# Kernel optimization log

Measured on AMD Instinct MI355X. Metric: run time of the kernel, lower is better.

The kernel has to match this reference:

```python
import jax, jax.numpy as jnp
import numpy as np

N_HEAD = 32
N_KV_HEAD = 8
HD = 64  # head dim
N_EMBD = 2048
B, T = 2, 2048
ROPE_THETA = 10000.0


def _apply_rope(x, cos, sin):
    # x: [B, T, H, HD]; cos/sin: [T, HD//2]. Interleaved complex pairs (even, odd),
    # matching torch.view_as_complex on x.reshape(..., -1, 2).
    x0 = x[..., 0::2]
    x1 = x[..., 1::2]
    c = cos[None, :, None, :]
    s = sin[None, :, None, :]
    o0 = x0 * c - x1 * s
    o1 = x0 * s + x1 * c
    return jnp.stack([o0, o1], axis=-1).reshape(x.shape)


def setup_inputs() -> dict:
    key = jax.random.key(0)
    k1, k2, k3 = jax.random.split(key, 3)
    x = jax.random.normal(k1, (B, T, N_EMBD), dtype=jnp.float32)
    Wqkv = jax.random.normal(k2, ((N_HEAD + 2 * N_KV_HEAD) * HD, N_EMBD), dtype=jnp.float32) * 0.02
    Wproj = jax.random.normal(k3, (N_EMBD, N_EMBD), dtype=jnp.float32) * 0.02
    # precompute_freqs_cis as in llm.c (llama path)
    freqs = 1.0 / (ROPE_THETA ** (np.arange(0, HD, 2, dtype=np.float32) / HD))
    ang = np.outer(np.arange(T, dtype=np.float32), freqs)  # [T, HD//2]
    freqs_cos = jnp.asarray(np.cos(ang), dtype=jnp.float32)
    freqs_sin = jnp.asarray(np.sin(ang), dtype=jnp.float32)
    return {"x": x, "Wqkv": Wqkv, "Wproj": Wproj,
            "freqs_cos": freqs_cos, "freqs_sin": freqs_sin, "start_pos": -1}


def reference(x, Wqkv, Wproj, freqs_cos, freqs_sin, start_pos):
    Bx, Tx, C = x.shape
    n_rep = N_HEAD // N_KV_HEAD
    qkv = x @ Wqkv.T  # [B, T, (H + 2*KV)*HD]
    q = qkv[..., : N_HEAD * HD].reshape(Bx, Tx, N_HEAD, HD)
    k = qkv[..., N_HEAD * HD: (N_HEAD + N_KV_HEAD) * HD].reshape(Bx, Tx, N_KV_HEAD, HD)
    v = qkv[..., (N_HEAD + N_KV_HEAD) * HD:].reshape(Bx, Tx, N_KV_HEAD, HD)
    # RoPE on q, k
    q = _apply_rope(q, freqs_cos, freqs_sin)
    k = _apply_rope(k, freqs_cos, freqs_sin)
    # start_pos < 0: training path, no KV cache. GQA repeat of kv heads.
    k = jnp.repeat(k, n_rep, axis=2)  # [B, T, H, HD]
    v = jnp.repeat(v, n_rep, axis=2)
    q = q.transpose(0, 2, 1, 3)  # [B, H, T, HD]
    k = k.transpose(0, 2, 1, 3)
    v = v.transpose(0, 2, 1, 3)
    scale = 1.0 / np.sqrt(HD).astype(np.float32)
    scores = jnp.einsum("bhtd,bhsd->bhts", q, k) * scale  # [B, H, T, T]
    causal = jnp.tril(jnp.ones((Tx, Tx), dtype=bool))
    scores = jnp.where(causal[None, None, :, :], scores, -jnp.inf)
    att = jax.nn.softmax(scores.astype(jnp.float32), axis=-1).astype(q.dtype)
    y = jnp.einsum("bhts,bhsd->bhtd", att, v)
    y = y.transpose(0, 2, 1, 3).reshape(Bx, Tx, C)
    return y @ Wproj.T
```

## Files before the change

### kernel.cpp

```cpp
#include <hip/hip_runtime.h>
#include <hip/hip_bf16.h>
#include <cstdint>

#define NH   32
#define NKV  8
#define HD   64
#define CE   2048
#define BB   2
#define TT   2048
#define QKVD 3072
#define MM   (BB*TT)

typedef float  f32x4  __attribute__((ext_vector_type(4)));
typedef float  f32x16 __attribute__((ext_vector_type(16)));
typedef short  s16x8  __attribute__((ext_vector_type(8)));
typedef unsigned short u16;

#define AS1 __attribute__((address_space(1)))
#define AS3 __attribute__((address_space(3)))
#define GLDS16(src, dst) __builtin_amdgcn_global_load_lds( \
    (const AS1 uint32_t*)(src), (AS3 uint32_t*)(dst), 16, 0, 0)

static __device__ __forceinline__ float bf2f(u16 u) {
    union { uint32_t u; float f; } v; v.u = ((uint32_t)u) << 16; return v.f;
}
static __device__ __forceinline__ u16 f2bf(float f) {
    union { float f; uint32_t u; } v; v.f = f;
    uint32_t r = v.u + 0x7fffu + ((v.u >> 16) & 1u);
    return (u16)(r >> 16);
}
static __device__ __forceinline__ uint32_t cvtpk(float lo, float hi) {
    uint32_t r;
    asm("v_cvt_pk_bf16_f32 %0, %1, %2" : "=v"(r) : "v"(lo), "v"(hi));
    return r;
}
static __device__ __forceinline__ void plswap(uint32_t &a, uint32_t &b) {
    asm volatile("v_permlane32_swap_b32 %0, %1" : "+v"(a), "+v"(b));
}

__global__ void k_f32_to_bf16(const float* __restrict__ in, uint32_t* __restrict__ out, int n8) {
    int i = blockIdx.x * blockDim.x + threadIdx.x;
    if (i >= n8) return;
    const float4* p = reinterpret_cast<const float4*>(in) + (size_t)i * 2;
    float4 a = p[0], b = p[1];
    uint4 o;
    o.x = cvtpk(a.x, a.y); o.y = cvtpk(a.z, a.w);
    o.z = cvtpk(b.x, b.y); o.w = cvtpk(b.z, b.w);
    *reinterpret_cast<uint4*>(out + (size_t)i * 4) = o;
}

template<bool OUT_BF16>
__global__ __launch_bounds__(256) void k_gemm_bt(const u16* __restrict__ A,
                                                 const u16* __restrict__ Bm,
                                                 void* __restrict__ Cout,
                                                 int M, int N, int K) {
    __shared__ u16 As[128 * 32];
    __shared__ u16 Bs[128 * 32];
    const int tid  = threadIdx.x;
    const int m0   = blockIdx.y * 128;
    const int n0   = blockIdx.x * 128;
    const int w    = tid >> 6;
    const int lane = tid & 63;
    const int lr   = lane & 15, lg = lane >> 4;
    const int wm   = (w >> 1) * 64, wn = (w & 1) * 64;

    const int o0 = w * 2048 + lane * 16, o1 = o0 + 1024;
    const int ar0 = o0 >> 6, ar1 = o1 >> 6;
    const int ac0 = (o0 & 63) >> 1, ac1 = (o1 & 63) >> 1;
    const size_t aof0 = (size_t)(m0 + ar0) * K + ac0;
    const size_t aof1 = (size_t)(m0 + ar1) * K + ac1;
    const size_t bof0 = (size_t)(n0 + ar0) * K + ac0;
    const size_t bof1 = (size_t)(n0 + ar1) * K + ac1;
    u16* dA0 = &As[w * 1024];       u16* dA1 = &As[w * 1024 + 512];
    u16* dB0 = &Bs[w * 1024];       u16* dB1 = &Bs[w * 1024 + 512];

    f32x4 acc[4][4] = {};

    for (int k0 = 0; k0 < K; k0 += 32) {
        GLDS16(A  + aof0 + k0, dA0);
        GLDS16(A  + aof1 + k0, dA1);
        GLDS16(Bm + bof0 + k0, dB0);
        GLDS16(Bm + bof1 + k0, dB1);
        __syncthreads();
        s16x8 af[4], bf[4];
        #pragma unroll
        for (int i = 0; i < 4; ++i)
            af[i] = *reinterpret_cast<const s16x8*>(&As[(wm + i * 16 + lr) * 32 + lg * 8]);
        #pragma unroll
        for (int j = 0; j < 4; ++j)
            bf[j] = *reinterpret_cast<const s16x8*>(&Bs[(wn + j * 16 + lr) * 32 + lg * 8]);
        #pragma unroll
        for (int i = 0; i < 4; ++i)
            #pragma unroll
            for (int j = 0; j < 4; ++j)
                acc[i][j] = __builtin_amdgcn_mfma_f32_16x16x32_bf16(af[i], bf[j], acc[i][j], 0, 0, 0);
        __syncthreads();
    }

    #pragma unroll
    for (int i = 0; i < 4; ++i)
        #pragma unroll
        for (int j = 0; j < 4; ++j)
            #pragma unroll
            for (int r = 0; r < 4; ++r) {
                int m = m0 + wm + i * 16 + lg * 4 + r;
                int n = n0 + wn + j * 16 + lr;
                if constexpr (OUT_BF16)
                    reinterpret_cast<u16*>(Cout)[(size_t)m * N + n] = f2bf(acc[i][j][r]);
                else
                    reinterpret_cast<float*>(Cout)[(size_t)m * N + n] = acc[i][j][r];
            }
}

__global__ void k_rope_scatter(const u16* __restrict__ qkv,
                               const float* __restrict__ fcos,
                               const float* __restrict__ fsin,
                               u16* __restrict__ Q,
                               u16* __restrict__ Kb,
                               u16* __restrict__ Vt) {
    int p = blockIdx.x * blockDim.x + threadIdx.x;
    if (p >= MM * (QKVD / 2)) return;
    int row = p / (QKVD / 2);
    int f   = (p % (QKVD / 2)) * 2;
    int b = row / TT, t = row % TT;
    uint32_t pk = reinterpret_cast<const uint32_t*>(qkv)[(size_t)row * (QKVD / 2) + (f >> 1)];
    u16 u0 = (u16)(pk & 0xffff), u1 = (u16)(pk >> 16);
    const float QS = 0.18033688011112042f;
    if (f < NH * HD) {
        int h = f / HD, d = f % HD;
        float c = fcos[t * 32 + (d >> 1)], s = fsin[t * 32 + (d >> 1)];
        float x0 = bf2f(u0), x1 = bf2f(u1);
        uint32_t o = cvtpk((x0 * c - x1 * s) * QS, (x0 * s + x1 * c) * QS);
        *reinterpret_cast<uint32_t*>(Q + ((size_t)((b * NH + h) * TT + t)) * HD + d) = o;
    } else if (f < NH * HD + NKV * HD) {
        int fk = f - NH * HD;
        int h = fk / HD, d = fk % HD;
        float c = fcos[t * 32 + (d >> 1)], s = fsin[t * 32 + (d >> 1)];
        float x0 = bf2f(u0), x1 = bf2f(u1);
        uint32_t o = cvtpk(x0 * c - x1 * s, x0 * s + x1 * c);
        *reinterpret_cast<uint32_t*>(Kb + ((size_t)((b * NKV + h) * TT + t)) * HD + d) = o;
    } else {
        int fv = f - NH * HD - NKV * HD;
        int h = fv / HD, d = fv % HD;
        Vt[((size_t)(b * NKV + h) * HD + d) * TT + t]     = u0;
        Vt[((size_t)(b * NKV + h) * HD + d + 1) * TT + t] = u1;
    }
}

__global__ __launch_bounds__(256) void k_attn(const u16* __restrict__ Q,
                                              const u16* __restrict__ Kb,
                                              const u16* __restrict__ Vt,
                                              u16* __restrict__ Y) {
    __shared__ u16 Ks[2][4096];
    __shared__ u16 Vs[2][4096];

    const int tid = threadIdx.x;
    const int w = tid >> 6, lane = tid & 63;
    const int ql = lane & 31, hi = lane >> 5;
    const int hi16 = hi << 4;
    const int b = blockIdx.z, h = blockIdx.y, kvh = h >> 2;

    const u16* qbase = Q  + ((size_t)(b * NH  + h  ) * TT) * HD;
    const u16* kbase = Kb + ((size_t)(b * NKV + kvh) * TT) * HD;
    const u16* vbase = Vt + ((size_t)(b * NKV + kvh) * HD) * TT;

    const int o0 = w * 2048 + lane * 16, o1 = o0 + 1024;
    const int r0 = o0 >> 7, r1 = o1 >> 7;
    const int c0 = (o0 & 127) ^ ((r0 & 7) << 4);
    const int c1 = (o1 & 127) ^ ((r1 & 7) << 4);
    const size_t kof0 = (size_t)r0 * HD + (c0 >> 1);
    const size_t kof1 = (size_t)r1 * HD + (c1 >> 1);
    const size_t vof0 = (size_t)r0 * TT + (c0 >> 1);
    const size_t vof1 = (size_t)r1 * TT + (c1 >> 1);

    const char* KsB = (const char*)&Ks[0][0];
    const char* VsB = (const char*)&Vs[0][0];
    const int krb0 = (0 * 32 + ql) * 128, ksz0 = ((0 * 32 + ql) & 7) << 4;
    const int krb1 = (1 * 32 + ql) * 128, ksz1 = ((1 * 32 + ql) & 7) << 4;

    #pragma unroll 1
    for (int pi = 0; pi < 2; ++pi) {
        const int j    = pi ? (int)blockIdx.x : (15 - (int)blockIdx.x);
        const int q0w  = j * 128 + w * 32;
        const int nt   = 2 * j + 2;
        const int tmxw = (q0w + 31) >> 6;
        const int qabs = q0w + ql;

        s16x8 qf[4];
        #pragma unroll
        for (int ds = 0; ds < 4; ++ds)
            qf[ds] = *reinterpret_cast<const s16x8*>(qbase + (size_t)qabs * HD + ds * 16 + 8 * hi);
        asm volatile("s_waitcnt vmcnt(0)" ::: "memory");

        GLDS16(kbase + kof0, &Ks[0][w * 1024]);
        GLDS16(kbase + kof1, &Ks[0][w * 1024 + 512]);
        GLDS16(vbase + vof0, &Vs[0][w * 1024]);
        GLDS16(vbase + vof1, &Vs[0][w * 1024 + 512]);

        float mrow = -1e30f, lrowp = 0.f;
        f32x16 oT0 = {}, oT1 = {};

        for (int t = 0; t < nt; ++t) {
            const int cur = t & 1;
            const int kv0 = t * 64;
            if (t + 1 < nt) {
                const size_t kb2 = (size_t)(kv0 + 64) * HD;
                GLDS16(kbase + kb2 + kof0, &Ks[cur ^ 1][w * 1024]);
                GLDS16(kbase + kb2 + kof1, &Ks[cur ^ 1][w * 1024 + 512]);
                GLDS16(vbase + (kv0 + 64) + vof0, &Vs[cur ^ 1][w * 1024]);
                GLDS16(vbase + (kv0 + 64) + vof1, &Vs[cur ^ 1][w * 1024 + 512]);
                asm volatile("s_waitcnt vmcnt(4)" ::: "memory");
            } else {
                asm volatile("s_waitcnt vmcnt(0)" ::: "memory");
            }
            __builtin_amdgcn_s_barrier();
            __builtin_amdgcn_sched_barrier(0);

            if (t <= tmxw) {
                const int bufo = cur * 8192;

                f32x16 sc0 = {}, sc1 = {};
                #pragma unroll
                for (int ds = 0; ds < 4; ++ds) {
                    s16x8 k0 = *reinterpret_cast<const s16x8*>(KsB + bufo + krb0 + (((ds << 5) | hi16) ^ ksz0));
                    s16x8 k1 = *reinterpret_cast<const s16x8*>(KsB + bufo + krb1 + (((ds << 5) | hi16) ^ ksz1));
                    sc0 = __builtin_amdgcn_mfma_f32_32x32x16_bf16(k0, qf[ds], sc0, 0, 0, 0);
                    sc1 = __builtin_amdgcn_mfma_f32_32x32x16_bf16(k1, qf[ds], sc1, 0, 0, 0);
                }

                float p0[16], p1[16];
                #pragma unroll
                for (int r = 0; r < 16; ++r) { p0[r] = sc0[r]; p1[r] = sc1[r]; }

                if (t == tmxw) {
                    const int dq = qabs - kv0 - 4 * hi;
                    #pragma unroll
                    for (int r = 0; r < 16; ++r) {
                        const int kr = (r & 3) + 8 * (r >> 2);
                        p0[r] = (kr      <= dq) ? p0[r] : -1e30f;
                        p1[r] = (kr + 32 <= dq) ? p1[r] : -1e30f;
                    }
                }

                float tmax = fmaxf(p0[0], p1[0]);
                #pragma unroll
                for (int r = 1; r < 16; ++r) tmax = fmaxf(tmax, fmaxf(p0[r], p1[r]));
                if (__any(tmax > mrow + 8.f)) {
                    float tf = fmaxf(tmax, __shfl_xor(tmax, 32, 64));
                    float mn = fmaxf(mrow, tf);
                    float alpha = __builtin_amdgcn_exp2f(mrow - mn);
                    mrow = mn;
                    lrowp *= alpha;
                    #pragma unroll
                    for (int r = 0; r < 16; ++r) { oT0[r] *= alpha; oT1[r] *= alpha; }
                }

                float sum = 0.f;
                #pragma unroll
                for (int r = 0; r < 16; ++r) {
                    p0[r] = __builtin_amdgcn_exp2f(p0[r] - mrow);
                    p1[r] = __builtin_amdgcn_exp2f(p1[r] - mrow);
                    sum += p0[r] + p1[r];
                }
                lrowp += sum;

                #pragma unroll
                for (int ks = 0; ks < 2; ++ks) {
                    uint32_t a0 = cvtpk(p0[ks * 8 + 0], p0[ks * 8 + 1]);
                    uint32_t b0 = cvtpk(p0[ks * 8 + 4], p0[ks * 8 + 5]);
                    plswap(a0, b0);
                    uint32_t a1 = cvtpk(p0[ks * 8 + 2], p0[ks * 8 + 3]);
                    uint32_t b1 = cvtpk(p0[ks * 8 + 6], p0[ks * 8 + 7]);
                    plswap(a1, b1);
                    union { uint32_t d[4]; s16x8 v; } pb;
                    pb.d[0] = a0; pb.d[1] = a1; pb.d[2] = b0; pb.d[3] = b1;
                    const int colb = (0 << 6) | (ks << 5) | hi16;
                    s16x8 v0 = *reinterpret_cast<const s16x8*>(VsB + bufo + krb0 + (colb ^ ksz0));
                    s16x8 v1 = *reinterpret_cast<const s16x8*>(VsB + bufo + krb1 + (colb ^ ksz1));
                    oT0 = __builtin_amdgcn_mfma_f32_32x32x16_bf16(v0, pb.v, oT0, 0, 0, 0);
                    oT1 = __builtin_amdgcn_mfma_f32_32x32x16_bf16(v1, pb.v, oT1, 0, 0, 0);
                }
                #pragma unroll
                for (int ks = 0; ks < 2; ++ks) {
                    uint32_t a0 = cvtpk(p1[ks * 8 + 0], p1[ks * 8 + 1]);
                    uint32_t b0 = cvtpk(p1[ks * 8 + 4], p1[ks * 8 + 5]);
                    plswap(a0, b0);
                    uint32_t a1 = cvtpk(p1[ks * 8 + 2], p1[ks * 8 + 3]);
                    uint32_t b1 = cvtpk(p1[ks * 8 + 6], p1[ks * 8 + 7]);
                    plswap(a1, b1);
                    union { uint32_t d[4]; s16x8 v; } pb;
                    pb.d[0] = a0; pb.d[1] = a1; pb.d[2] = b0; pb.d[3] = b1;
                    const int colb = (1 << 6) | (ks << 5) | hi16;
                    s16x8 v0 = *reinterpret_cast<const s16x8*>(VsB + bufo + krb0 + (colb ^ ksz0));
                    s16x8 v1 = *reinterpret_cast<const s16x8*>(VsB + bufo + krb1 + (colb ^ ksz1));
                    oT0 = __builtin_amdgcn_mfma_f32_32x32x16_bf16(v0, pb.v, oT0, 0, 0, 0);
                    oT1 = __builtin_amdgcn_mfma_f32_32x32x16_bf16(v1, pb.v, oT1, 0, 0, 0);
                }
            }

            __builtin_amdgcn_sched_barrier(0);
            __builtin_amdgcn_s_barrier();
        }

        lrowp += __shfl_xor(lrowp, 32, 64);
        const float rinv = 1.f / lrowp;
        const size_t yrow = ((size_t)(b * TT + qabs) * NH + h) * HD;
        #pragma unroll
        for (int rp = 0; rp < 8; ++rp) {
            const int d = ((2 * rp) & 3) + 8 * (rp >> 1) + 4 * hi;
            *reinterpret_cast<uint32_t*>(Y + yrow + d) =
                cvtpk(oT0[2 * rp] * rinv, oT0[2 * rp + 1] * rinv);
            *reinterpret_cast<uint32_t*>(Y + yrow + 32 + d) =
                cvtpk(oT1[2 * rp] * rinv, oT1[2 * rp + 1] * rinv);
        }
    }
}

extern "C" void kernel_launch(void* const* d_in, const int* in_sizes, int n_in,
                              void* d_out, int out_size, void* d_ws, size_t ws_size,
                              hipStream_t stream) {
    (void)in_sizes; (void)n_in; (void)out_size; (void)ws_size;
    const float* x     = (const float*)d_in[0];
    const float* wqkv  = (const float*)d_in[1];
    const float* wproj = (const float*)d_in[2];
    const float* fcos  = (const float*)d_in[3];
    const float* fsin  = (const float*)d_in[4];

    char* ws = (char*)d_ws;
    size_t off = 0;
    auto alloc = [&](size_t bytes) { void* p = ws + off; off += (bytes + 255) & ~(size_t)255; return p; };
    u16* Xbf  = (u16*)alloc((size_t)MM * CE * 2);
    u16* Wqb  = (u16*)alloc((size_t)QKVD * CE * 2);
    u16* Wpb  = (u16*)alloc((size_t)CE * CE * 2);
    u16* QKVb = (u16*)alloc((size_t)MM * QKVD * 2);
    u16* Qb   = (u16*)alloc((size_t)BB * NH * TT * HD * 2);
    u16* Kbuf = (u16*)alloc((size_t)BB * NKV * TT * HD * 2);
    u16* Vtb  = (u16*)alloc((size_t)BB * NKV * HD * TT * 2);
    u16* Yb   = (u16*)alloc((size_t)MM * CE * 2);

    k_f32_to_bf16<<<(MM * CE / 8 + 255) / 256, 256, 0, stream>>>(x, (uint32_t*)Xbf, MM * CE / 8);
    k_f32_to_bf16<<<(QKVD * CE / 8 + 255) / 256, 256, 0, stream>>>(wqkv, (uint32_t*)Wqb, QKVD * CE / 8);
    k_f32_to_bf16<<<(CE * CE / 8 + 255) / 256, 256, 0, stream>>>(wproj, (uint32_t*)Wpb, CE * CE / 8);

    dim3 g1(QKVD / 128, MM / 128);
    k_gemm_bt<true><<<g1, 256, 0, stream>>>(Xbf, Wqb, QKVb, MM, QKVD, CE);

    int pairs = MM * (QKVD / 2);
    k_rope_scatter<<<(pairs + 255) / 256, 256, 0, stream>>>(QKVb, fcos, fsin, Qb, Kbuf, Vtb);

    dim3 ga(8, NH, BB);
    k_attn<<<ga, 256, 0, stream>>>(Qb, Kbuf, Vtb, Yb);

    dim3 g2(CE / 128, MM / 128);
    k_gemm_bt<false><<<g2, 256, 0, stream>>>(Yb, Wpb, d_out, MM, CE, CE);
}
```

Measured before the change: 238.8 us.

## Fuse RoPE and QKV scatter into QKV GEMM epilogue, remap tiles, add setprio

Moves RoPE, Q scaling and the Q/K/Vt scatter into the epilogue of the QKV GEMM, which removes the intermediate QKV buffer and the separate rope/scatter kernel. Both GEMMs now remap block indices so that tiles sharing the same A rows run close together, for better L2 reuse. The attention kernel also wraps its MFMA sections in s_setprio so those waves get issue priority. The cost is an epilogue with lane shuffles and scattered cos/sin loads inside the GEMM.

```diff
diff --git a/kernel.cpp b/kernel.cpp
--- a/kernel.cpp
+++ b/kernel.cpp
@@ -49,16 +49,22 @@
     *reinterpret_cast<uint4*>(out + (size_t)i * 4) = o;
 }
 
-template<bool OUT_BF16>
-__global__ __launch_bounds__(256) void k_gemm_bt(const u16* __restrict__ A,
-                                                 const u16* __restrict__ Bm,
-                                                 void* __restrict__ Cout,
-                                                 int M, int N, int K) {
+__global__ __launch_bounds__(256) void k_gemm_qkv(const u16* __restrict__ A,
+                                                  const u16* __restrict__ Bm,
+                                                  u16* __restrict__ Qb,
+                                                  u16* __restrict__ Kb,
+                                                  u16* __restrict__ Vt,
+                                                  const float* __restrict__ fcos,
+                                                  const float* __restrict__ fsin) {
     __shared__ u16 As[128 * 32];
     __shared__ u16 Bs[128 * 32];
+    const int K = CE;
+    const int c  = blockIdx.x + 24 * blockIdx.y;
+    const int nc = (c & 7) * 96 + (c >> 3);
+    const int m0 = (nc / 24) * 128;
+    const int n0 = (nc % 24) * 128;
+
     const int tid  = threadIdx.x;
-    const int m0   = blockIdx.y * 128;
-    const int n0   = blockIdx.x * 128;
     const int w    = tid >> 6;
     const int lane = tid & 63;
     const int lr   = lane & 15, lg = lane >> 4;
@@ -97,6 +103,106 @@
         __syncthreads();
     }
 
+    const float QS = 0.18033688011112042f;
+    const int bb = m0 / TT;
+    const int tb = m0 - bb * TT + wm;
+    #pragma unroll
+    for (int i = 0; i < 4; ++i) {
+        const int t0 = tb + i * 16 + lg * 4;
+        #pragma unroll
+        for (int j = 0; j < 4; ++j) {
+            const int n = n0 + wn + j * 16 + lr;
+            if (n0 < NH * HD) {
+                const int hh = n >> 6, d = n & 63;
+                #pragma unroll
+                for (int r = 0; r < 4; ++r) {
+                    const int t = t0 + r;
+                    const float cc = fcos[t * 32 + (d >> 1)];
+                    const float ss = fsin[t * 32 + (d >> 1)];
+                    float v = acc[i][j][r];
+                    float p = __shfl_xor(v, 1, 64);
+                    float o = ((lr & 1) ? (p * ss + v * cc) : (v * cc - p * ss)) * QS;
+                    float po = __shfl_xor(o, 1, 64);
+                    if (!(lr & 1))
+                        *reinterpret_cast<uint32_t*>(Qb + ((size_t)((bb * NH + hh) * TT + t)) * HD + d) = cvtpk(o, po);
+                }
+            } else if (n0 < (NH + NKV) * HD) {
+                const int fk = n - NH * HD;
+                const int hh = fk >> 6, d = fk & 63;
+                #pragma unroll
+                for (int r = 0; r < 4; ++r) {
+                    const int t = t0 + r;
+                    const float cc = fcos[t * 32 + (d >> 1)];
+                    const float ss = fsin[t * 32 + (d >> 1)];
+                    float v = acc[i][j][r];
+                    float p = __shfl_xor(v, 1, 64);
+                    float o = (lr & 1) ? (p * ss + v * cc) : (v * cc - p * ss);
+                    float po = __shfl_xor(o, 1, 64);
+                    if (!(lr & 1))
+                        *reinterpret_cast<uint32_t*>(Kb + ((size_t)((bb * NKV + hh) * TT + t)) * HD + d) = cvtpk(o, po);
+                }
+            } else {
+                const int fv = n - (NH + NKV) * HD;
+                const int vh = fv >> 6, d = fv & 63;
+                uint2 st;
+                st.x = cvtpk(acc[i][j][0], acc[i][j][1]);
+                st.y = cvtpk(acc[i][j][2], acc[i][j][3]);
+                *reinterpret_cast<uint2*>(Vt + ((size_t)(bb * NKV + vh) * HD + d) * TT + t0) = st;
+            }
+        }
+    }
+}
+
+__global__ __launch_bounds__(256) void k_gemm_bt(const u16* __restrict__ A,
+                                                 const u16* __restrict__ Bm,
+                                                 float* __restrict__ Cout,
+                                                 int M, int N, int K) {
+    __shared__ u16 As[128 * 32];
+    __shared__ u16 Bs[128 * 32];
+    const int c  = blockIdx.x + 16 * blockIdx.y;
+    const int nc = (c & 7) * 64 + (c >> 3);
+    const int m0 = (nc >> 4) * 128;
+    const int n0 = (nc & 15) * 128;
+
+    const int tid  = threadIdx.x;
+    const int w    = tid >> 6;
+    const int lane = tid & 63;
+    const int lr   = lane & 15, lg = lane >> 4;
+    const int wm   = (w >> 1) * 64, wn = (w & 1) * 64;
+
+    const int o0 = w * 2048 + lane * 16, o1 = o0 + 1024;
+    const int ar0 = o0 >> 6, ar1 = o1 >> 6;
+    const int ac0 = (o0 & 63) >> 1, ac1 = (o1 & 63) >> 1;
+    const size_t aof0 = (size_t)(m0 + ar0) * K + ac0;
+    const size_t aof1 = (size_t)(m0 + ar1) * K + ac1;
+    const size_t bof0 = (size_t)(n0 + ar0) * K + ac0;
+    const size_t bof1 = (size_t)(n0 + ar1) * K + ac1;
+    u16* dA0 = &As[w * 1024];       u16* dA1 = &As[w * 1024 + 512];
+    u16* dB0 = &Bs[w * 1024];       u16* dB1 = &Bs[w * 1024 + 512];
+
+    f32x4 acc[4][4] = {};
+
+    for (int k0 = 0; k0 < K; k0 += 32) {
+        GLDS16(A  + aof0 + k0, dA0);
+        GLDS16(A  + aof1 + k0, dA1);
+        GLDS16(Bm + bof0 + k0, dB0);
+        GLDS16(Bm + bof1 + k0, dB1);
+        __syncthreads();
+        s16x8 af[4], bf[4];
+        #pragma unroll
+        for (int i = 0; i < 4; ++i)
+            af[i] = *reinterpret_cast<const s16x8*>(&As[(wm + i * 16 + lr) * 32 + lg * 8]);
+        #pragma unroll
+        for (int j = 0; j < 4; ++j)
+            bf[j] = *reinterpret_cast<const s16x8*>(&Bs[(wn + j * 16 + lr) * 32 + lg * 8]);
+        #pragma unroll
+        for (int i = 0; i < 4; ++i)
+            #pragma unroll
+            for (int j = 0; j < 4; ++j)
+                acc[i][j] = __builtin_amdgcn_mfma_f32_16x16x32_bf16(af[i], bf[j], acc[i][j], 0, 0, 0);
+        __syncthreads();
+    }
+
     #pragma unroll
     for (int i = 0; i < 4; ++i)
         #pragma unroll
@@ -105,46 +211,8 @@
             for (int r = 0; r < 4; ++r) {
                 int m = m0 + wm + i * 16 + lg * 4 + r;
                 int n = n0 + wn + j * 16 + lr;
-                if constexpr (OUT_BF16)
-                    reinterpret_cast<u16*>(Cout)[(size_t)m * N + n] = f2bf(acc[i][j][r]);
-                else
-                    reinterpret_cast<float*>(Cout)[(size_t)m * N + n] = acc[i][j][r];
+                Cout[(size_t)m * N + n] = acc[i][j][r];
             }
-}
-
-__global__ void k_rope_scatter(const u16* __restrict__ qkv,
-                               const float* __restrict__ fcos,
-                               const float* __restrict__ fsin,
-                               u16* __restrict__ Q,
-                               u16* __restrict__ Kb,
-                               u16* __restrict__ Vt) {
-    int p = blockIdx.x * blockDim.x + threadIdx.x;
-    if (p >= MM * (QKVD / 2)) return;
-    int row = p / (QKVD / 2);
-    int f   = (p % (QKVD / 2)) * 2;
-    int b = row / TT, t = row % TT;
-    uint32_t pk = reinterpret_cast<const uint32_t*>(qkv)[(size_t)row * (QKVD / 2) + (f >> 1)];
-    u16 u0 = (u16)(pk & 0xffff), u1 = (u16)(pk >> 16);
-    const float QS = 0.18033688011112042f;
-    if (f < NH * HD) {
-        int h = f / HD, d = f % HD;
-        float c = fcos[t * 32 + (d >> 1)], s = fsin[t * 32 + (d >> 1)];
-        float x0 = bf2f(u0), x1 = bf2f(u1);
-        uint32_t o = cvtpk((x0 * c - x1 * s) * QS, (x0 * s + x1 * c) * QS);
-        *reinterpret_cast<uint32_t*>(Q + ((size_t)((b * NH + h) * TT + t)) * HD + d) = o;
-    } else if (f < NH * HD + NKV * HD) {
-        int fk = f - NH * HD;
-        int h = fk / HD, d = fk % HD;
-        float c = fcos[t * 32 + (d >> 1)], s = fsin[t * 32 + (d >> 1)];
-        float x0 = bf2f(u0), x1 = bf2f(u1);
-        uint32_t o = cvtpk(x0 * c - x1 * s, x0 * s + x1 * c);
-        *reinterpret_cast<uint32_t*>(Kb + ((size_t)((b * NKV + h) * TT + t)) * HD + d) = o;
-    } else {
-        int fv = f - NH * HD - NKV * HD;
-        int h = fv / HD, d = fv % HD;
-        Vt[((size_t)(b * NKV + h) * HD + d) * TT + t]     = u0;
-        Vt[((size_t)(b * NKV + h) * HD + d + 1) * TT + t] = u1;
-    }
 }
 
 __global__ __launch_bounds__(256) void k_attn(const u16* __restrict__ Q,
@@ -220,6 +288,7 @@
                 const int bufo = cur * 8192;
 
                 f32x16 sc0 = {}, sc1 = {};
+                __builtin_amdgcn_s_setprio(1);
                 #pragma unroll
                 for (int ds = 0; ds < 4; ++ds) {
                     s16x8 k0 = *reinterpret_cast<const s16x8*>(KsB + bufo + krb0 + (((ds << 5) | hi16) ^ ksz0));
@@ -227,6 +296,7 @@
                     sc0 = __builtin_amdgcn_mfma_f32_32x32x16_bf16(k0, qf[ds], sc0, 0, 0, 0);
                     sc1 = __builtin_amdgcn_mfma_f32_32x32x16_bf16(k1, qf[ds], sc1, 0, 0, 0);
                 }
+                __builtin_amdgcn_s_setprio(0);
 
                 float p0[16], p1[16];
                 #pragma unroll
@@ -264,6 +334,7 @@
                 }
                 lrowp += sum;
 
+                __builtin_amdgcn_s_setprio(1);
                 #pragma unroll
                 for (int ks = 0; ks < 2; ++ks) {
                     uint32_t a0 = cvtpk(p0[ks * 8 + 0], p0[ks * 8 + 1]);
@@ -296,6 +367,7 @@
                     oT0 = __builtin_amdgcn_mfma_f32_32x32x16_bf16(v0, pb.v, oT0, 0, 0, 0);
                     oT1 = __builtin_amdgcn_mfma_f32_32x32x16_bf16(v1, pb.v, oT1, 0, 0, 0);
                 }
+                __builtin_amdgcn_s_setprio(0);
             }
 
             __builtin_amdgcn_sched_barrier(0);
@@ -332,7 +404,6 @@
     u16* Xbf  = (u16*)alloc((size_t)MM * CE * 2);
     u16* Wqb  = (u16*)alloc((size_t)QKVD * CE * 2);
     u16* Wpb  = (u16*)alloc((size_t)CE * CE * 2);
-    u16* QKVb = (u16*)alloc((size_t)MM * QKVD * 2);
     u16* Qb   = (u16*)alloc((size_t)BB * NH * TT * HD * 2);
     u16* Kbuf = (u16*)alloc((size_t)BB * NKV * TT * HD * 2);
     u16* Vtb  = (u16*)alloc((size_t)BB * NKV * HD * TT * 2);
@@ -343,14 +414,11 @@
     k_f32_to_bf16<<<(CE * CE / 8 + 255) / 256, 256, 0, stream>>>(wproj, (uint32_t*)Wpb, CE * CE / 8);
 
     dim3 g1(QKVD / 128, MM / 128);
-    k_gemm_bt<true><<<g1, 256, 0, stream>>>(Xbf, Wqb, QKVb, MM, QKVD, CE);
-
-    int pairs = MM * (QKVD / 2);
-    k_rope_scatter<<<(pairs + 255) / 256, 256, 0, stream>>>(QKVb, fcos, fsin, Qb, Kbuf, Vtb);
+    k_gemm_qkv<<<g1, 256, 0, stream>>>(Xbf, Wqb, Qb, Kbuf, Vtb, fcos, fsin);
 
     dim3 ga(8, NH, BB);
     k_attn<<<ga, 256, 0, stream>>>(Qb, Kbuf, Vtb, Yb);
 
     dim3 g2(CE / 128, MM / 128);
-    k_gemm_bt<false><<<g2, 256, 0, stream>>>(Yb, Wpb, d_out, MM, CE, CE);
-}
+    k_gemm_bt<<<g2, 256, 0, stream>>>(Yb, Wpb, (float*)d_out, MM, CE, CE);
+}
```

New measurement: 215.4 us. 9.8% less time.
